# Kernel optimization log

Measured on AMD Instinct MI355X. Metric: run time of the kernel, lower is better.

The kernel has to match this reference:

```python
import jax, jax.numpy as jnp
import numpy as np

B, T, C = 2048, 200, 128
PAD = jnp.float32(-4294967295.0)  # -(2**32) + 1, as in SoftmaxWeightedSum padding


def setup_inputs() -> dict:
    key = jax.random.key(0)
    k1, k2, k3, k4 = jax.random.split(key, 4)
    user_query = jax.random.normal(k1, (B, 1, C), dtype=jnp.float32)
    keys = jax.random.normal(k2, (B, T, C), dtype=jnp.float32)
    keys_length = jax.random.randint(k3, (B, 1), 0, T, dtype=jnp.int32)
    W = jax.random.normal(k4, (C, C), dtype=jnp.float32) * (1.0 / np.sqrt(C))
    b = jnp.zeros((C,), dtype=jnp.float32)
    return {"user_query": user_query, "keys": keys, "keys_length": keys_length, "W": W, "b": b}


def reference(user_query, keys, keys_length, W, b):
    # Dense with tanh activation: [B,1,C] -> [B,1,C]
    query = jnp.tanh(jnp.einsum('bqc,cd->bqd', user_query, W) + b)
    # DotAttention with scale: [B,1,T]
    scale = jnp.asarray(1.0 / np.sqrt(C), dtype=keys.dtype)
    align = jnp.einsum('bqc,btc->bqt', query, keys) * scale
    # sequence mask [B,1,T] from keys_length [B,1]
    key_masks = jnp.arange(T, dtype=keys_length.dtype)[None, None, :] < keys_length[:, :, None]
    align = jnp.where(key_masks, align, PAD)
    align = jax.nn.softmax(align, axis=-1)
    # weighted sum over history: [B,1,C]
    output = jnp.einsum('bqt,btc->bqc', align, keys)
    # residual: broadcasts [B,1,C] + [B,T,C] -> [B,T,C] (faithful to `output += keys`)
    output = output + keys
    # mean pool over sequence, keepdims -> [B,1,C]
    return jnp.mean(output, axis=1, keepdims=True)
```

## Files before the change

kernel.cpp:

```cpp
#include <hip/hip_runtime.h>
#include <hip/hip_bf16.h>
#include <math.h>

#define BB 2048
#define TT 200
#define CC 128
#define PADV (-4294967295.0f)
#define SCALE 0.08838834764831845f
#define INVT (1.0f / 200.0f)
#define PITCH 132

__global__ __launch_bounds__(512) void user_attn_kernel(
    const float* __restrict__ uq,
    const float* __restrict__ keys,
    const int*   __restrict__ klen,
    const float* __restrict__ W,
    const float* __restrict__ bias,
    float*       __restrict__ out)
{
    const int b    = blockIdx.x;
    const int tid  = threadIdx.x;
    const int lane = tid & 63;
    const int wid  = tid >> 6;

    __shared__ unsigned short s_kb16[TT * PITCH];
    __shared__ float s_q[CC];
    __shared__ float s_w[TT];
    __shared__ float s_tmp[16];

    float*  s_part = (float*)s_kb16;
    float*  s_uq   = (float*)s_kb16 + 512;
    float4* s_red  = (float4*)s_kb16;

    const float* kb = keys + (size_t)b * TT * CC;

    if (tid < CC) s_uq[tid] = uq[b * CC + tid];
    __syncthreads();
    {
        const int d    = tid & 127;
        const int part = tid >> 7;
        float acc = 0.0f;
        const int c0 = part * 32;
        #pragma unroll 8
        for (int c = 0; c < 32; ++c)
            acc = fmaf(s_uq[c0 + c], W[(c0 + c) * CC + d], acc);
        s_part[part * CC + d] = acc;
    }
    __syncthreads();
    if (tid < CC) {
        float acc = bias[tid] + s_part[tid] + s_part[CC + tid]
                  + s_part[2 * CC + tid] + s_part[3 * CC + tid];
        s_q[tid] = tanhf(acc);
    }
    __syncthreads();

    const int len = klen[b];

    const int cl = lane & 31;
    const int c4 = cl * 4;
    const int h  = lane >> 5;
    const float q0 = s_q[c4], q1 = s_q[c4 + 1], q2 = s_q[c4 + 2], q3 = s_q[c4 + 3];

    for (int p = wid; p < TT / 2; p += 8) {
        const int r = 2 * p + h;
        const float4 k = *(const float4*)(kb + r * CC + c4);
        float d = q0 * k.x + q1 * k.y + q2 * k.z + q3 * k.w;
        #pragma unroll
        for (int off = 1; off < 32; off <<= 1)
            d += __shfl_xor(d, off, 64);
        if (cl == 0)
            s_w[r] = (r < len) ? d * SCALE : PADV;

        __hip_bfloat16 h0 = __float2bfloat16(k.x);
        __hip_bfloat16 h1 = __float2bfloat16(k.y);
        __hip_bfloat16 h2 = __float2bfloat16(k.z);
        __hip_bfloat16 h3 = __float2bfloat16(k.w);
        ushort4 pk;
        pk.x = *(unsigned short*)&h0; pk.y = *(unsigned short*)&h1;
        pk.z = *(unsigned short*)&h2; pk.w = *(unsigned short*)&h3;
        *(ushort4*)(&s_kb16[(size_t)r * PITCH + c4]) = pk;
    }
    __syncthreads();

    {
        float v = (tid < TT) ? s_w[tid] : -INFINITY;
        float m = v;
        #pragma unroll
        for (int off = 1; off < 64; off <<= 1)
            m = fmaxf(m, __shfl_xor(m, off, 64));
        if (lane == 0) s_tmp[wid] = m;
        __syncthreads();
        m = s_tmp[0];
        #pragma unroll
        for (int w = 1; w < 8; ++w) m = fmaxf(m, s_tmp[w]);

        float e = (tid < TT) ? expf(v - m) : 0.0f;
        float ssum = e;
        #pragma unroll
        for (int off = 1; off < 64; off <<= 1)
            ssum += __shfl_xor(ssum, off, 64);
        if (lane == 0) s_tmp[8 + wid] = ssum;
        __syncthreads();
        ssum = 0.0f;
        #pragma unroll
        for (int w = 0; w < 8; ++w) ssum += s_tmp[8 + w];
        if (tid < TT) s_w[tid] = e / ssum + INVT;
    }
    __syncthreads();

    float4 acc = make_float4(0.0f, 0.0f, 0.0f, 0.0f);
    for (int p = wid; p < TT / 2; p += 8) {
        const int r = 2 * p + h;
        const float w = s_w[r];
        const ushort4 pk = *(const ushort4*)(&s_kb16[(size_t)r * PITCH + c4]);
        acc.x = fmaf(w, __uint_as_float((unsigned)pk.x << 16), acc.x);
        acc.y = fmaf(w, __uint_as_float((unsigned)pk.y << 16), acc.y);
        acc.z = fmaf(w, __uint_as_float((unsigned)pk.z << 16), acc.z);
        acc.w = fmaf(w, __uint_as_float((unsigned)pk.w << 16), acc.w);
    }
    acc.x += __shfl_xor(acc.x, 32, 64);
    acc.y += __shfl_xor(acc.y, 32, 64);
    acc.z += __shfl_xor(acc.z, 32, 64);
    acc.w += __shfl_xor(acc.w, 32, 64);

    __syncthreads();
    if (cl == lane)
        s_red[wid * 32 + cl] = acc;
    __syncthreads();

    if (tid < 32) {
        float4 r = s_red[tid];
        #pragma unroll
        for (int w = 1; w < 8; ++w) {
            float4 v = s_red[w * 32 + tid];
            r.x += v.x; r.y += v.y; r.z += v.z; r.w += v.w;
        }
        *(float4*)(out + (size_t)b * CC + 4 * tid) = r;
    }
}

extern "C" void kernel_launch(void* const* d_in, const int* in_sizes, int n_in,
                              void* d_out, int out_size, void* d_ws, size_t ws_size,
                              hipStream_t stream) {
    const float* uq   = (const float*)d_in[0];
    const float* keys = (const float*)d_in[1];
    const int*   klen = (const int*)d_in[2];
    const float* W    = (const float*)d_in[3];
    const float* bias = (const float*)d_in[4];
    float* out = (float*)d_out;

    user_attn_kernel<<<BB, 512, 0, stream>>>(uq, keys, klen, W, bias, out);
}
```

Baseline: 306.2 us.

## Split query GEMV into separate kernel and stream keys to LDS before scoring

Moves the per-batch dense+tanh query computation into its own kernel that writes to workspace, so the attention kernel starts immediately by streaming all keys into LDS as truncated bf16 with fully coalesced loads. Scores are then computed per row from LDS instead of with warp shuffles over global loads. Also changes rounding to truncation and adds an occupancy hint to the launch bounds. The gain depends on hiding key-load latency better; it adds a second launch, a global round trip for q, and slightly lower precision from truncation.

```diff
diff --git a/kernel.cpp b/kernel.cpp
--- a/kernel.cpp
+++ b/kernel.cpp
@@ -1,5 +1,4 @@
 #include <hip/hip_runtime.h>
-#include <hip/hip_bf16.h>
 #include <math.h>
 
 #define BB 2048
@@ -10,12 +9,37 @@
 #define INVT (1.0f / 200.0f)
 #define PITCH 132
 
-__global__ __launch_bounds__(512) void user_attn_kernel(
+__device__ __forceinline__ float bf2f(unsigned short u) {
+    return __uint_as_float((unsigned)u << 16);
+}
+
+__global__ __launch_bounds__(256) void q_gemv_kernel(
     const float* __restrict__ uq,
+    const float* __restrict__ W,
+    const float* __restrict__ bias,
+    float*       __restrict__ qws)
+{
+    const int tid = threadIdx.x;
+    const int d   = tid & 127;
+    const int wh  = tid >> 7;
+    const int b   = blockIdx.x * 2 + wh;
+
+    __shared__ float s_uq[2 * CC];
+    s_uq[tid] = uq[blockIdx.x * 2 * CC + tid];
+    __syncthreads();
+
+    float acc = bias[d];
+    const float* uqr = &s_uq[wh * CC];
+    #pragma unroll 16
+    for (int c = 0; c < CC; ++c)
+        acc = fmaf(uqr[c], W[c * CC + d], acc);
+    qws[(size_t)b * CC + d] = tanhf(acc);
+}
+
+__global__ __launch_bounds__(512, 6) void attn_main_kernel(
     const float* __restrict__ keys,
     const int*   __restrict__ klen,
-    const float* __restrict__ W,
-    const float* __restrict__ bias,
+    const float* __restrict__ qws,
     float*       __restrict__ out)
 {
     const int b    = blockIdx.x;
@@ -23,62 +47,58 @@
     const int lane = tid & 63;
     const int wid  = tid >> 6;
 
-    __shared__ unsigned short s_kb16[TT * PITCH];
+    __shared__ unsigned short s_k[TT * PITCH];
     __shared__ float s_q[CC];
     __shared__ float s_w[TT];
     __shared__ float s_tmp[16];
+    float4* s_red = (float4*)s_k;
 
-    float*  s_part = (float*)s_kb16;
-    float*  s_uq   = (float*)s_kb16 + 512;
-    float4* s_red  = (float4*)s_kb16;
+    const float*  kb = keys + (size_t)b * TT * CC;
+    const float4* gp = (const float4*)kb + tid;
 
-    const float* kb = keys + (size_t)b * TT * CC;
+    if (tid < CC) s_q[tid] = qws[(size_t)b * CC + tid];
+    const int len = klen[b];
 
-    if (tid < CC) s_uq[tid] = uq[b * CC + tid];
-    __syncthreads();
     {
-        const int d    = tid & 127;
-        const int part = tid >> 7;
-        float acc = 0.0f;
-        const int c0 = part * 32;
-        #pragma unroll 8
-        for (int c = 0; c < 32; ++c)
-            acc = fmaf(s_uq[c0 + c], W[(c0 + c) * CC + d], acc);
-        s_part[part * CC + d] = acc;
-    }
-    __syncthreads();
-    if (tid < CC) {
-        float acc = bias[tid] + s_part[tid] + s_part[CC + tid]
-                  + s_part[2 * CC + tid] + s_part[3 * CC + tid];
-        s_q[tid] = tanhf(acc);
+        const int r0 = tid >> 5;
+        const int cq = tid & 31;
+        const int l0 = r0 * PITCH + cq * 4;
+        #pragma unroll 4
+        for (int i = 0; i < 12; ++i) {
+            const float4 k = gp[512 * i];
+            ushort4 pk;
+            pk.x = (unsigned short)(__float_as_uint(k.x) >> 16);
+            pk.y = (unsigned short)(__float_as_uint(k.y) >> 16);
+            pk.z = (unsigned short)(__float_as_uint(k.z) >> 16);
+            pk.w = (unsigned short)(__float_as_uint(k.w) >> 16);
+            *(ushort4*)&s_k[l0 + i * 16 * PITCH] = pk;
+        }
+        if (tid < 256) {
+            const float4 k = gp[512 * 12];
+            ushort4 pk;
+            pk.x = (unsigned short)(__float_as_uint(k.x) >> 16);
+            pk.y = (unsigned short)(__float_as_uint(k.y) >> 16);
+            pk.z = (unsigned short)(__float_as_uint(k.z) >> 16);
+            pk.w = (unsigned short)(__float_as_uint(k.w) >> 16);
+            *(ushort4*)&s_k[l0 + 12 * 16 * PITCH] = pk;
+        }
     }
     __syncthreads();
 
-    const int len = klen[b];
-
-    const int cl = lane & 31;
-    const int c4 = cl * 4;
-    const int h  = lane >> 5;
-    const float q0 = s_q[c4], q1 = s_q[c4 + 1], q2 = s_q[c4 + 2], q3 = s_q[c4 + 3];
-
-    for (int p = wid; p < TT / 2; p += 8) {
-        const int r = 2 * p + h;
-        const float4 k = *(const float4*)(kb + r * CC + c4);
-        float d = q0 * k.x + q1 * k.y + q2 * k.z + q3 * k.w;
-        #pragma unroll
-        for (int off = 1; off < 32; off <<= 1)
-            d += __shfl_xor(d, off, 64);
-        if (cl == 0)
-            s_w[r] = (r < len) ? d * SCALE : PADV;
-
-        __hip_bfloat16 h0 = __float2bfloat16(k.x);
-        __hip_bfloat16 h1 = __float2bfloat16(k.y);
-        __hip_bfloat16 h2 = __float2bfloat16(k.z);
-        __hip_bfloat16 h3 = __float2bfloat16(k.w);
-        ushort4 pk;
-        pk.x = *(unsigned short*)&h0; pk.y = *(unsigned short*)&h1;
-        pk.z = *(unsigned short*)&h2; pk.w = *(unsigned short*)&h3;
-        *(ushort4*)(&s_kb16[(size_t)r * PITCH + c4]) = pk;
+    if (tid < TT) {
+        const ushort4* rowp = (const ushort4*)&s_k[tid * PITCH];
+        float a0 = 0.f, a1 = 0.f, a2 = 0.f, a3 = 0.f;
+        #pragma unroll 8
+        for (int j = 0; j < 32; ++j) {
+            const ushort4 pk = rowp[j];
+            const float* qj = &s_q[4 * j];
+            a0 = fmaf(qj[0], bf2f(pk.x), a0);
+            a1 = fmaf(qj[1], bf2f(pk.y), a1);
+            a2 = fmaf(qj[2], bf2f(pk.z), a2);
+            a3 = fmaf(qj[3], bf2f(pk.w), a3);
+        }
+        const float d = (a0 + a1) + (a2 + a3);
+        s_w[tid] = (tid < len) ? d * SCALE : PADV;
     }
     __syncthreads();
 
@@ -108,15 +128,17 @@
     }
     __syncthreads();
 
-    float4 acc = make_float4(0.0f, 0.0f, 0.0f, 0.0f);
+    const int cl = lane & 31;
+    const int h  = lane >> 5;
+    float4 acc = make_float4(0.f, 0.f, 0.f, 0.f);
     for (int p = wid; p < TT / 2; p += 8) {
         const int r = 2 * p + h;
         const float w = s_w[r];
-        const ushort4 pk = *(const ushort4*)(&s_kb16[(size_t)r * PITCH + c4]);
-        acc.x = fmaf(w, __uint_as_float((unsigned)pk.x << 16), acc.x);
-        acc.y = fmaf(w, __uint_as_float((unsigned)pk.y << 16), acc.y);
-        acc.z = fmaf(w, __uint_as_float((unsigned)pk.z << 16), acc.z);
-        acc.w = fmaf(w, __uint_as_float((unsigned)pk.w << 16), acc.w);
+        const ushort4 pk = *(const ushort4*)&s_k[r * PITCH + cl * 4];
+        acc.x = fmaf(w, bf2f(pk.x), acc.x);
+        acc.y = fmaf(w, bf2f(pk.y), acc.y);
+        acc.z = fmaf(w, bf2f(pk.z), acc.z);
+        acc.w = fmaf(w, bf2f(pk.w), acc.w);
     }
     acc.x += __shfl_xor(acc.x, 32, 64);
     acc.y += __shfl_xor(acc.y, 32, 64);
@@ -124,15 +146,14 @@
     acc.w += __shfl_xor(acc.w, 32, 64);
 
     __syncthreads();
-    if (cl == lane)
-        s_red[wid * 32 + cl] = acc;
+    if (h == 0) s_red[wid * 32 + cl] = acc;
     __syncthreads();
 
     if (tid < 32) {
         float4 r = s_red[tid];
         #pragma unroll
         for (int w = 1; w < 8; ++w) {
-            float4 v = s_red[w * 32 + tid];
+            const float4 v = s_red[w * 32 + tid];
             r.x += v.x; r.y += v.y; r.z += v.z; r.w += v.w;
         }
         *(float4*)(out + (size_t)b * CC + 4 * tid) = r;
@@ -148,6 +169,8 @@
     const float* W    = (const float*)d_in[3];
     const float* bias = (const float*)d_in[4];
     float* out = (float*)d_out;
+    float* qws = (float*)d_ws;
 
-    user_attn_kernel<<<BB, 512, 0, stream>>>(uq, keys, klen, W, bias, out);
+    q_gemv_kernel<<<BB / 2, 256, 0, stream>>>(uq, W, bias, qws);
+    attn_main_kernel<<<BB, 512, 0, stream>>>(keys, klen, qws, out);
 }
```

Result: no change. 303.0 us (-1.1%).
